# Kernel optimization log

Hardware: AMD Instinct MI355X
Metric: run time of the kernel (lower is better)

## Reference

```python
import jax, jax.numpy as jnp
import numpy as np

N, EMB, ATT = 65536, 1024, 512


def setup_inputs() -> dict:
    key = jax.random.key(0)
    k = jax.random.split(key, 6)
    scale = 0.02
    return {
        "leaves": jax.random.normal(k[0], (N, EMB), dtype=jnp.float32),
        "ancestors": jax.random.normal(k[1], (N, EMB), dtype=jnp.float32),
        "W1": jax.random.normal(k[2], (2 * EMB, ATT), dtype=jnp.float32) * scale,
        "b1": jax.random.normal(k[3], (ATT,), dtype=jnp.float32) * scale,
        "W2": jax.random.normal(k[4], (ATT, 1), dtype=jnp.float32) * scale,
        "b2": jax.random.normal(k[5], (1,), dtype=jnp.float32) * scale,
    }


def reference(leaves, ancestors, W1, b1, W2, b2):
    # concat -> [N, 2*EMB]
    x = jnp.concatenate([leaves, ancestors], axis=-1)
    # additive attention MLP: linear -> tanh -> linear -> [N, 1]
    h = jnp.tanh(x @ W1 + b1)
    scores = h @ W2 + b2            # [N, 1]
    attn = jax.nn.softmax(scores, axis=0)  # softmax over the pair dim
    # reshape to [1, N], matmul ancestors [N, EMB] -> [1, EMB], sum dim 0 -> [EMB]
    out = jnp.squeeze(attn, axis=1) @ ancestors  # [EMB]
    return out
```

## Files before the change

kernel.cpp:

```cpp
#include <hip/hip_runtime.h>
#include <hip/hip_bf16.h>
#include <stdint.h>
#include <stddef.h>

typedef __bf16 bf16;
typedef bf16 bf16x8 __attribute__((ext_vector_type(8)));
typedef float f32x4 __attribute__((ext_vector_type(4)));

#define N_ROWS 65536
#define EMB    1024
#define ATTD   512
#define KDIM   2048
#define BM     128
#define BN     128
#define BK     64
#define NKB    (KDIM / BK)
#define MBLK   (N_ROWS / BM)
#define NSPL   (ATTD / BN)

__device__ __forceinline__ void gload_lds16(const void* g, void* l) {
  __builtin_amdgcn_global_load_lds(
      (const __attribute__((address_space(1))) void*)g,
      (__attribute__((address_space(3))) void*)l, 16, 0, 0);
}

__global__ __launch_bounds__(256) void k_prep_w1(const float* __restrict__ W1,
                                                 bf16* __restrict__ W1t) {
  __shared__ float tile[64][132];
  const int kb = blockIdx.x;
  const int bn = blockIdx.y;
  const int t  = threadIdx.x;

  const int kr = t >> 2;
  const int nc = (t & 3) * 32;
  const float* src = W1 + (size_t)(kb * 64 + kr) * ATTD + bn * 128 + nc;
  #pragma unroll
  for (int q = 0; q < 8; ++q) {
    float4 v = *(const float4*)(src + q * 4);
    tile[kr][nc + q * 4 + 0] = v.x;
    tile[kr][nc + q * 4 + 1] = v.y;
    tile[kr][nc + q * 4 + 2] = v.z;
    tile[kr][nc + q * 4 + 3] = v.w;
  }
  __syncthreads();

  const int nl = t >> 1;
  const int pb = (t & 1) * 4;
  bf16* dst = W1t + (size_t)(kb * 4 + bn) * (BN * BK);
  #pragma unroll
  for (int pi = 0; pi < 4; ++pi) {
    const int p = pb + pi;
    const int c = p ^ (nl & 7);
    bf16x8 o;
    #pragma unroll
    for (int e = 0; e < 8; ++e) o[e] = (bf16)tile[c * 8 + e][nl];
    *(bf16x8*)(dst + ((size_t)nl * 8 + p) * 8) = o;
  }
}

__global__ __launch_bounds__(256, 3) void k_gemm_score(
    const float* __restrict__ leaves, const float* __restrict__ anc,
    const bf16* __restrict__ W1t, const float* __restrict__ b1,
    const float* __restrict__ W2, float* __restrict__ spart) {
  __shared__ float ldsAf[BM * BK];
  __shared__ bf16  ldsB[BN * BK];

  const int t    = threadIdx.x;
  const int lane = t & 63;
  const int wave = t >> 6;
  const int l15  = lane & 15;
  const int l4   = lane >> 4;
  const int wm2  = wave >> 1;
  const int wn2  = wave & 1;

  const int g   = blockIdx.x;
  const int sb  = g >> 5;
  const int q   = g & 31;
  const int bn  = q >> 3;
  const int bm  = sb * 8 + (q & 7);
  const int m0  = bm * BM;
  const int n0  = bn * BN;

  const int a_rbase = t >> 4;
  const int a_lpair = ((t >> 1) & 7) ^ ((t >> 4) & 7);
  const int a_koff  = a_lpair * 8 + (t & 1) * 4;

  const f32x4 zero4 = {0.f, 0.f, 0.f, 0.f};
  f32x4 acc[4][4];
  #pragma unroll
  for (int i = 0; i < 4; ++i)
    #pragma unroll
    for (int j = 0; j < 4; ++j) acc[i][j] = zero4;

  for (int kb = 0; kb < NKB; ++kb) {
    const bf16* Bsrc = W1t + (size_t)(kb * 4 + bn) * (BN * BK);
    #pragma unroll
    for (int j = 0; j < 4; ++j)
      gload_lds16(Bsrc + ((size_t)(wave * 4 + j) * 64 + lane) * 8,
                  ldsB + (wave * 4 + j) * 512);
    const float* Abase = (kb < 16)
        ? leaves + (size_t)m0 * EMB + (size_t)kb * BK
        : anc    + (size_t)m0 * EMB + (size_t)(kb - 16) * BK;
    #pragma unroll
    for (int s = 0; s < 8; ++s) {
      const int r = s * 16 + a_rbase;
      gload_lds16(Abase + (size_t)r * EMB + a_koff,
                  ldsAf + (s * 256 + t) * 4);
    }
    __syncthreads();
    #pragma unroll
    for (int ks = 0; ks < 2; ++ks) {
      bf16x8 af[4], bfr[4];
      #pragma unroll
      for (int mi = 0; mi < 4; ++mi) {
        const int row   = wm2 * 64 + mi * 16 + l15;
        const int ppair = (ks * 4 + l4) ^ (row & 7);
        const float* ap = ldsAf + row * BK + ppair * 8;
        f32x4 lo = *(const f32x4*)(ap);
        f32x4 hi = *(const f32x4*)(ap + 4);
        af[mi] = (bf16x8){(bf16)lo.x, (bf16)lo.y, (bf16)lo.z, (bf16)lo.w,
                          (bf16)hi.x, (bf16)hi.y, (bf16)hi.z, (bf16)hi.w};
      }
      #pragma unroll
      for (int ni = 0; ni < 4; ++ni) {
        const int nrow = wn2 * 64 + ni * 16 + l15;
        const int p    = (ks * 4 + l4) ^ (nrow & 7);
        bfr[ni] = *(const bf16x8*)(ldsB + nrow * BK + p * 8);
      }
      #pragma unroll
      for (int ni = 0; ni < 4; ++ni)
        #pragma unroll
        for (int mi = 0; mi < 4; ++mi)
          acc[mi][ni] = __builtin_amdgcn_mfma_f32_16x16x32_bf16(
              af[mi], bfr[ni], acc[mi][ni], 0, 0, 0);
    }
    __syncthreads();
  }

  float b1c[4], w2c[4];
  #pragma unroll
  for (int ni = 0; ni < 4; ++ni) {
    const int col = n0 + wn2 * 64 + ni * 16 + l15;
    b1c[ni] = b1[col];
    w2c[ni] = W2[col];
  }
  float* sp = ldsAf;
  #pragma unroll
  for (int mi = 0; mi < 4; ++mi) {
    #pragma unroll
    for (int r = 0; r < 4; ++r) {
      float p = 0.f;
      #pragma unroll
      for (int ni = 0; ni < 4; ++ni)
        p += tanhf(acc[mi][ni][r] + b1c[ni]) * w2c[ni];
      p += __shfl_xor(p, 1);
      p += __shfl_xor(p, 2);
      p += __shfl_xor(p, 4);
      p += __shfl_xor(p, 8);
      if (l15 == 0) sp[wn2 * 128 + wm2 * 64 + mi * 16 + l4 * 4 + r] = p;
    }
  }
  __syncthreads();
  if (t < BM)
    spart[(size_t)bn * N_ROWS + m0 + t] = sp[t] + sp[128 + t];
}

__global__ __launch_bounds__(128) void k_combine(
    const float* __restrict__ spart, const float* __restrict__ b2,
    float* __restrict__ scores, float* __restrict__ bmax,
    float* __restrict__ bsum) {
  const int b = blockIdx.x, t = threadIdx.x;
  const int lane = t & 63, wave = t >> 6;
  const int m = b * 128 + t;
  __shared__ float rm[2], rs[2];
  const float s = spart[m] + spart[N_ROWS + m] + spart[2 * N_ROWS + m] +
                  spart[3 * N_ROWS + m] + b2[0];
  scores[m] = s;
  float mm = s;
  #pragma unroll
  for (int o = 32; o; o >>= 1) mm = fmaxf(mm, __shfl_xor(mm, o));
  if (lane == 0) rm[wave] = mm;
  __syncthreads();
  const float bM = fmaxf(rm[0], rm[1]);
  float ee = __expf(s - bM);
  #pragma unroll
  for (int o = 32; o; o >>= 1) ee += __shfl_xor(ee, o);
  if (lane == 0) rs[wave] = ee;
  __syncthreads();
  if (t == 0) {
    bmax[b] = bM;
    bsum[b] = rs[0] + rs[1];
  }
}

__global__ __launch_bounds__(512) void k_mz(const float* __restrict__ bmax,
                                            const float* __restrict__ bsum,
                                            float* __restrict__ MZ,
                                            float* __restrict__ scale) {
  const int t = threadIdx.x, lane = t & 63, wave = t >> 6;
  __shared__ float rm[8], rs[8];
  const float m = bmax[t];
  float mm = m;
  #pragma unroll
  for (int o = 32; o; o >>= 1) mm = fmaxf(mm, __shfl_xor(mm, o));
  if (lane == 0) rm[wave] = mm;
  __syncthreads();
  if (t == 0) {
    float g = rm[0];
    for (int i = 1; i < 8; ++i) g = fmaxf(g, rm[i]);
    rm[0] = g;
  }
  __syncthreads();
  const float M = rm[0];
  const float sc = __expf(m - M);
  scale[t] = sc;
  float z = bsum[t] * sc;
  #pragma unroll
  for (int o = 32; o; o >>= 1) z += __shfl_xor(z, o);
  if (lane == 0) rs[wave] = z;
  __syncthreads();
  if (t == 0) {
    float Z = 0.f;
    for (int i = 0; i < 8; ++i) Z += rs[i];
    MZ[0] = M;
    MZ[1] = Z;
  }
}

__global__ __launch_bounds__(256) void k_part(const float* __restrict__ anc,
                                              const float* __restrict__ scores,
                                              const float* __restrict__ bmax,
                                              float* __restrict__ part) {
  __shared__ float w[BM];
  const int b = blockIdx.x, t = threadIdx.x;
  const float bM = bmax[b];
  if (t < BM) w[t] = __expf(scores[(size_t)b * BM + t] - bM);
  __syncthreads();
  float4 a = {0.f, 0.f, 0.f, 0.f};
  const float4* src = (const float4*)(anc + (size_t)b * BM * EMB) + t;
  #pragma unroll 4
  for (int i = 0; i < BM; ++i) {
    float4 v = src[i * (EMB / 4)];
    const float wi = w[i];
    a.x += wi * v.x;
    a.y += wi * v.y;
    a.z += wi * v.z;
    a.w += wi * v.w;
  }
  ((float4*)(part + (size_t)b * EMB))[t] = a;
}

__global__ __launch_bounds__(256) void k_final(const float* __restrict__ part,
                                               const float* __restrict__ scale,
                                               const float* __restrict__ MZ,
                                               float* __restrict__ out) {
  const int j = blockIdx.x * 256 + threadIdx.x;
  float s0 = 0.f, s1 = 0.f, s2 = 0.f, s3 = 0.f;
  for (int b = 0; b < MBLK; b += 4) {
    s0 += part[(size_t)(b + 0) * EMB + j] * scale[b + 0];
    s1 += part[(size_t)(b + 1) * EMB + j] * scale[b + 1];
    s2 += part[(size_t)(b + 2) * EMB + j] * scale[b + 2];
    s3 += part[(size_t)(b + 3) * EMB + j] * scale[b + 3];
  }
  out[j] = (s0 + s1 + s2 + s3) / MZ[1];
}

extern "C" void kernel_launch(void* const* d_in, const int* in_sizes, int n_in,
                              void* d_out, int out_size, void* d_ws,
                              size_t ws_size, hipStream_t stream) {
  const float* leaves = (const float*)d_in[0];
  const float* anc    = (const float*)d_in[1];
  const float* W1     = (const float*)d_in[2];
  const float* b1     = (const float*)d_in[3];
  const float* W2     = (const float*)d_in[4];
  const float* b2     = (const float*)d_in[5];
  float* out = (float*)d_out;

  char* ws = (char*)d_ws;
  bf16*  W1t    = (bf16*)ws;
  float* spart  = (float*)(ws + (2u << 20));
  float* scores = (float*)(ws + (3u << 20));
  float* bmax   = (float*)(ws + (3u << 20) + (1u << 18));
  float* bsum   = bmax + MBLK;
  float* scale  = bsum + MBLK;
  float* MZ     = scale + MBLK;
  float* part   = (float*)(ws + (4u << 20));

  k_prep_w1<<<dim3(32, 4), 256, 0, stream>>>(W1, W1t);
  k_gemm_score<<<dim3(MBLK * NSPL), 256, 0, stream>>>(leaves, anc, W1t, b1, W2,
                                                      spart);
  k_combine<<<dim3(MBLK), 128, 0, stream>>>(spart, b2, scores, bmax, bsum);
  k_mz<<<dim3(1), 512, 0, stream>>>(bmax, bsum, MZ, scale);
  k_part<<<dim3(MBLK), 256, 0, stream>>>(anc, scores, bmax, part);
  k_final<<<dim3(EMB / 256), 256, 0, stream>>>(part, scale, MZ, out);
}
```

Baseline: 290.4 us.

## Double-buffer GEMM tiles with register-staged A converted to bf16 before LDS

Replaces the single-buffered fp32 A tile in LDS with a double-buffered bf16 A and B layout. A is loaded into registers for the next k-block, then converted and written to LDS after the current block's MFMAs, while B for the next block is prefetched directly into the other buffer. This overlaps global loads with compute, halves A's LDS footprint and removes the per-fragment fp32-to-bf16 conversions from the inner loop. In exchange it raises register pressure, and occupancy is lowered from 3 to 2 blocks per SIMD.

```diff
diff --git a/kernel.cpp b/kernel.cpp
--- a/kernel.cpp
+++ b/kernel.cpp
@@ -58,12 +58,12 @@
   }
 }
 
-__global__ __launch_bounds__(256, 3) void k_gemm_score(
+__global__ __launch_bounds__(256, 2) void k_gemm_score(
     const float* __restrict__ leaves, const float* __restrict__ anc,
     const bf16* __restrict__ W1t, const float* __restrict__ b1,
     const float* __restrict__ W2, float* __restrict__ spart) {
-  __shared__ float ldsAf[BM * BK];
-  __shared__ bf16  ldsB[BN * BK];
+  __shared__ bf16 ldsA[2][BM * BK];
+  __shared__ bf16 ldsB[2][BN * BK];
 
   const int t    = threadIdx.x;
   const int lane = t & 63;
@@ -81,9 +81,27 @@
   const int m0  = bm * BM;
   const int n0  = bn * BN;
 
-  const int a_rbase = t >> 4;
-  const int a_lpair = ((t >> 1) & 7) ^ ((t >> 4) & 7);
-  const int a_koff  = a_lpair * 8 + (t & 1) * 4;
+  const int ar = t >> 1;
+  const int c0 = (t & 1) * 4;
+  int a_wr[4];
+  #pragma unroll
+  for (int i = 0; i < 4; ++i)
+    a_wr[i] = ar * BK + ((c0 + i) ^ (ar & 7)) * 8;
+
+  int a_rd[2][4], b_rd[2][4];
+  #pragma unroll
+  for (int ks = 0; ks < 2; ++ks) {
+    #pragma unroll
+    for (int mi = 0; mi < 4; ++mi) {
+      const int row = wm2 * 64 + mi * 16 + l15;
+      a_rd[ks][mi] = row * BK + ((ks * 4 + l4) ^ (row & 7)) * 8;
+    }
+    #pragma unroll
+    for (int ni = 0; ni < 4; ++ni) {
+      const int nrow = wn2 * 64 + ni * 16 + l15;
+      b_rd[ks][ni] = nrow * BK + ((ks * 4 + l4) ^ (nrow & 7)) * 8;
+    }
+  }
 
   const f32x4 zero4 = {0.f, 0.f, 0.f, 0.f};
   f32x4 acc[4][4];
@@ -92,41 +110,56 @@
     #pragma unroll
     for (int j = 0; j < 4; ++j) acc[i][j] = zero4;
 
-  for (int kb = 0; kb < NKB; ++kb) {
+  float4 rA[8];
+
+  auto issueB = [&](int kb, int buf) {
     const bf16* Bsrc = W1t + (size_t)(kb * 4 + bn) * (BN * BK);
     #pragma unroll
     for (int j = 0; j < 4; ++j)
       gload_lds16(Bsrc + ((size_t)(wave * 4 + j) * 64 + lane) * 8,
-                  ldsB + (wave * 4 + j) * 512);
-    const float* Abase = (kb < 16)
-        ? leaves + (size_t)m0 * EMB + (size_t)kb * BK
-        : anc    + (size_t)m0 * EMB + (size_t)(kb - 16) * BK;
-    #pragma unroll
-    for (int s = 0; s < 8; ++s) {
-      const int r = s * 16 + a_rbase;
-      gload_lds16(Abase + (size_t)r * EMB + a_koff,
-                  ldsAf + (s * 256 + t) * 4);
-    }
-    __syncthreads();
+                  &ldsB[buf][(wave * 4 + j) * 512]);
+  };
+  auto loadA = [&](int kb) {
+    const float* Ap = ((kb < 16)
+        ? leaves + (size_t)(m0 + ar) * EMB + (size_t)kb * BK
+        : anc    + (size_t)(m0 + ar) * EMB + (size_t)(kb - 16) * BK)
+        + c0 * 8;
+    #pragma unroll
+    for (int qi = 0; qi < 8; ++qi)
+      rA[qi] = *(const float4*)(Ap + qi * 4);
+  };
+  auto writeA = [&](int buf) {
+    #pragma unroll
+    for (int i = 0; i < 4; ++i) {
+      const float4 va = rA[2 * i], vb = rA[2 * i + 1];
+      bf16x8 o = {(bf16)va.x, (bf16)va.y, (bf16)va.z, (bf16)va.w,
+                  (bf16)vb.x, (bf16)vb.y, (bf16)vb.z, (bf16)vb.w};
+      *(bf16x8*)(&ldsA[buf][a_wr[i]]) = o;
+    }
+  };
+
+  issueB(0, 0);
+  loadA(0);
+  writeA(0);
+  __syncthreads();
+
+  for (int kb = 0; kb < NKB; ++kb) {
+    const int cur = kb & 1, nxt = cur ^ 1;
+    const bool pf = (kb + 1 < NKB);
+    if (pf) {
+      issueB(kb + 1, nxt);
+      loadA(kb + 1);
+    }
+    __builtin_amdgcn_sched_barrier(0);
     #pragma unroll
     for (int ks = 0; ks < 2; ++ks) {
       bf16x8 af[4], bfr[4];
       #pragma unroll
-      for (int mi = 0; mi < 4; ++mi) {
-        const int row   = wm2 * 64 + mi * 16 + l15;
-        const int ppair = (ks * 4 + l4) ^ (row & 7);
-        const float* ap = ldsAf + row * BK + ppair * 8;
-        f32x4 lo = *(const f32x4*)(ap);
-        f32x4 hi = *(const f32x4*)(ap + 4);
-        af[mi] = (bf16x8){(bf16)lo.x, (bf16)lo.y, (bf16)lo.z, (bf16)lo.w,
-                          (bf16)hi.x, (bf16)hi.y, (bf16)hi.z, (bf16)hi.w};
-      }
+      for (int mi = 0; mi < 4; ++mi)
+        af[mi] = *(const bf16x8*)(&ldsA[cur][a_rd[ks][mi]]);
       #pragma unroll
-      for (int ni = 0; ni < 4; ++ni) {
-        const int nrow = wn2 * 64 + ni * 16 + l15;
-        const int p    = (ks * 4 + l4) ^ (nrow & 7);
-        bfr[ni] = *(const bf16x8*)(ldsB + nrow * BK + p * 8);
-      }
+      for (int ni = 0; ni < 4; ++ni)
+        bfr[ni] = *(const bf16x8*)(&ldsB[cur][b_rd[ks][ni]]);
       #pragma unroll
       for (int ni = 0; ni < 4; ++ni)
         #pragma unroll
@@ -134,6 +167,8 @@
           acc[mi][ni] = __builtin_amdgcn_mfma_f32_16x16x32_bf16(
               af[mi], bfr[ni], acc[mi][ni], 0, 0, 0);
     }
+    __builtin_amdgcn_sched_barrier(0);
+    if (pf) writeA(nxt);
     __syncthreads();
   }
 
@@ -144,7 +179,7 @@
     b1c[ni] = b1[col];
     w2c[ni] = W2[col];
   }
-  float* sp = ldsAf;
+  float* sp = (float*)&ldsA[0][0];
   #pragma unroll
   for (int mi = 0; mi < 4; ++mi) {
     #pragma unroll
```

Result: slower. 476.4 us (+64.1%).
